# Performance work log

Hardware: AMD Instinct MI355X
Metric: run time of the kernel (lower is better)

Reference implementation:

```python
import jax, jax.numpy as jnp
import numpy as np

B, H, W, L, C = 4, 64, 64, 64, 64
NB, BS, F = 8, 8, 1          # num_blocks, block_size, hidden_size_factor
R, ALPHA = 8, 1.0            # lora_r, lora_alpha
M, T = 32, 8                 # modes, temporal_modes
SCALE = 1.0 / (BS * BS * F)  # param init scale from the module


def setup_inputs() -> dict:
    key = jax.random.key(0)
    ks = jax.random.split(key, 14)
    d = {"x": jax.random.normal(ks[0], (B, H, W, L, C), jnp.float32)}
    d["w1"] = SCALE * jax.random.uniform(ks[1], (2, NB, BS, BS * F), jnp.float32)
    d["b1"] = SCALE * jax.random.uniform(ks[2], (2, NB, BS * F), jnp.float32)
    d["w2"] = SCALE * jax.random.uniform(ks[3], (2, NB, BS * F, BS), jnp.float32)
    d["b2"] = SCALE * jax.random.uniform(ks[4], (2, NB, BS), jnp.float32)
    names = ["la1rA", "la1rB", "la1iA", "la1iB", "la2rA", "la2rB", "la2iA", "la2iB"]
    shapes = [(NB, BS, R), (NB, R, BS * F), (NB, BS, R), (NB, R, BS * F),
              (NB, BS * F, R), (NB, R, BS), (NB, BS * F, R), (NB, R, BS)]
    for i, (n, s) in enumerate(zip(names, shapes)):
        d[n] = 0.02 * jax.random.normal(ks[5 + i], s, jnp.float32)
    return d


def _afno(x, w1, b1, w2, b2, la1rA, la1rB, la1iA, la1iB, la2rA, la2rB, la2iA, la2iB):
    s = ALPHA / R
    # effective per-block weights: base + LoRA low-rank update  [NB, in, out]
    W1r = w1[0] + s * jnp.einsum('nir,nro->nio', la1rA, la1rB)
    W1i = w1[1] + s * jnp.einsum('nir,nro->nio', la1iA, la1iB)
    W2r = w2[0] + s * jnp.einsum('nir,nro->nio', la2rA, la2rB)
    W2i = w2[1] + s * jnp.einsum('nir,nro->nio', la2iA, la2iB)

    xf = jnp.fft.rfftn(x, axes=(1, 2, 3), norm='ortho')      # [B,H,W,L//2+1,C] complex
    Lh = xf.shape[3]
    xs = xf[:, :M, :M, :T].reshape(B, M, M, T, NB, BS)        # truncated modes, block split
    xr, xi = xs.real, xs.imag

    def lin(v, Wb, bb):  # block-diagonal linear: [...,n,i] x [n,i,o] + [n,o]
        return jnp.einsum('bxyzni,nio->bxyzno', v, Wb) + bb

    gelu = lambda t: jax.nn.gelu(t, approximate=False)
    o1r = gelu(lin(xr, W1r, b1[0]) - lin(xi, W1i, b1[1]))
    o1i = gelu(lin(xi, W1r, b1[0]) + lin(xr, W1i, b1[1]))
    o2r = lin(o1r, W2r, b2[0]) - lin(o1i, W2i, b2[1])
    o2i = lin(o1i, W2r, b2[0]) + lin(o1r, W2i, b2[1])

    o2 = (o2r + 1j * o2i).reshape(B, M, M, T, C)
    full = jnp.zeros((B, H, W, Lh, C), dtype=xf.dtype).at[:, :M, :M, :T].set(o2)
    out = jnp.fft.irfftn(full, s=(H, W, L), axes=(1, 2, 3), norm='ortho')
    return out + x


def reference(x, w1, b1, w2, b2, la1rA, la1rB, la1iA, la1iB, la2rA, la2rB, la2iA, la2iB):
    return _afno(x, w1, b1, w2, b2, la1rA, la1rB, la1iA, la1iB, la2rA, la2rB, la2iA, la2iB)
```

## Files before the change

kernel.cpp:

```cpp
#include <hip/hip_runtime.h>
#include <math.h>


#define PI2_64 0.09817477042468103f

__device__ __forceinline__ float gelu_exact(float t) {
    return 0.5f * t * (1.0f + erff(t * 0.7071067811865475f));
}

__global__ void __launch_bounds__(256) k1a_dft_l(const float* __restrict__ x,
                                                 float* __restrict__ y1f) {
    __shared__ float2 twT[8][64];
    int tid = threadIdx.x;
    {
        int k = tid >> 6, l = tid & 63;
        float s, c;
        sincosf(PI2_64 * (float)((k * l) & 63), &s, &c);
        twT[k][l] = make_float2(c, s);
        int k2 = k + 4;
        sincosf(PI2_64 * (float)((k2 * l) & 63), &s, &c);
        twT[k2][l] = make_float2(c, s);
    }
    __syncthreads();

    int bid = blockIdx.x;
    int w8 = bid & 7, bh = bid >> 3;
    int cp = tid & 31, wl = tid >> 5;
    int w = w8 * 8 + wl;
    const float* xp = x + (size_t)(bh * 64 + w) * 4096 + 2 * cp;

    float4 A[8];
#pragma unroll
    for (int kl = 0; kl < 8; ++kl) A[kl] = make_float4(0.f, 0.f, 0.f, 0.f);

    for (int l0 = 0; l0 < 64; l0 += 4) {
        float2 v0 = *(const float2*)(xp + (l0 + 0) * 64);
        float2 v1 = *(const float2*)(xp + (l0 + 1) * 64);
        float2 v2 = *(const float2*)(xp + (l0 + 2) * 64);
        float2 v3 = *(const float2*)(xp + (l0 + 3) * 64);
#pragma unroll
        for (int kl = 0; kl < 8; ++kl) {
            float2 t0 = twT[kl][l0 + 0];
            float2 t1 = twT[kl][l0 + 1];
            float2 t2 = twT[kl][l0 + 2];
            float2 t3 = twT[kl][l0 + 3];
            A[kl].x += v0.x * t0.x;  A[kl].y -= v0.x * t0.y;
            A[kl].z += v0.y * t0.x;  A[kl].w -= v0.y * t0.y;
            A[kl].x += v1.x * t1.x;  A[kl].y -= v1.x * t1.y;
            A[kl].z += v1.y * t1.x;  A[kl].w -= v1.y * t1.y;
            A[kl].x += v2.x * t2.x;  A[kl].y -= v2.x * t2.y;
            A[kl].z += v2.y * t2.x;  A[kl].w -= v2.y * t2.y;
            A[kl].x += v3.x * t3.x;  A[kl].y -= v3.x * t3.y;
            A[kl].z += v3.y * t3.x;  A[kl].w -= v3.y * t3.y;
        }
    }
    float4* y1 = (float4*)y1f;
    size_t base = (size_t)bh * 16384 + (size_t)w * 32 + cp;
#pragma unroll
    for (int kl = 0; kl < 8; ++kl)
        y1[base + kl * 2048] = A[kl];
}

__global__ void __launch_bounds__(256) k1b_dft_w(const float* __restrict__ y1f,
                                                 float* __restrict__ y2f) {
    __shared__ float4 sD[64 * 32];
    __shared__ float2 twT[32][64];
    int tid = threadIdx.x;
#pragma unroll
    for (int e = 0; e < 8; ++e) {
        int idx = e * 256 + tid;
        int k = idx >> 6, l = idx & 63;
        float s, c;
        sincosf(PI2_64 * (float)((k * l) & 63), &s, &c);
        twT[k][l] = make_float2(c, s);
    }
    int pos = blockIdx.x;
    int kl = pos & 7, bh = pos >> 3;
    const float4* src = (const float4*)y1f + (size_t)pos * 2048;
#pragma unroll
    for (int r = 0; r < 8; ++r)
        sD[r * 256 + tid] = src[r * 256 + tid];
    __syncthreads();

    int cp = tid & 31, kwg = tid >> 5;
    float4 acc[4];
#pragma unroll
    for (int i = 0; i < 4; ++i) acc[i] = make_float4(0.f, 0.f, 0.f, 0.f);

    for (int w = 0; w < 64; ++w) {
        float4 d = sD[w * 32 + cp];
#pragma unroll
        for (int i = 0; i < 4; ++i) {
            float2 t = twT[kwg * 4 + i][w];
            acc[i].x += d.x * t.x + d.y * t.y;
            acc[i].y += d.y * t.x - d.x * t.y;
            acc[i].z += d.z * t.x + d.w * t.y;
            acc[i].w += d.w * t.x - d.z * t.y;
        }
    }
    int b = bh >> 6, h = bh & 63;
    float4* y2 = (float4*)y2f;
#pragma unroll
    for (int i = 0; i < 4; ++i) {
        int kw = kwg * 4 + i;
        y2[((size_t)((b * 8 + kl) * 32 + kw) * 64 + h) * 32 + cp] = acc[i];
    }
}

__global__ void __launch_bounds__(256) kc_h_mlp(
        const float* __restrict__ y2f, float* __restrict__ z2f,
        const float* __restrict__ w1, const float* __restrict__ b1,
        const float* __restrict__ w2, const float* __restrict__ b2,
        const float* __restrict__ la1rA, const float* __restrict__ la1rB,
        const float* __restrict__ la1iA, const float* __restrict__ la1iB,
        const float* __restrict__ la2rA, const float* __restrict__ la2rB,
        const float* __restrict__ la2iA, const float* __restrict__ la2iB) {
    __shared__ float2 sD[64][64];
    __shared__ float2 sT[64][34];
    __shared__ float2 sM[32][66];
    __shared__ float  sW[4][512];
    __shared__ float  sb1[128], sb2[128];
    int tid = threadIdx.x;
    int pos = blockIdx.x;
    int kl = pos & 7, kw = (pos >> 3) & 31, b = pos >> 8;

#pragma unroll
    for (int r = 0; r < 8; ++r) {
        int idx = r * 256 + tid;
        int h = idx >> 5, kh = idx & 31;
        float sn, cs;
        sincosf(PI2_64 * (float)((h * kh) & 63), &sn, &cs);
        sT[h][kh] = make_float2(cs, -sn);
    }
    const float2* src = (const float2*)y2f + (size_t)((b * 8 + kl) * 32 + kw) * 4096;
#pragma unroll
    for (int r = 0; r < 8; ++r) {
        int f = r * 512 + tid * 2;
        *(float4*)(&sD[f >> 6][f & 63]) = *(const float4*)(src + f);
    }
    {
        const float* As[4]   = {la1rA, la1iA, la2rA, la2iA};
        const float* Bs[4]   = {la1rB, la1iB, la2rB, la2iB};
        const float* base[4] = {w1, w1 + 512, w2, w2 + 512};
#pragma unroll
        for (int e = 0; e < 8; ++e) {
            int flat = tid + e * 256;
            int mat = flat >> 9;
            int rem = flat & 511;
            int n = rem >> 6, i = (rem >> 3) & 7, o = rem & 7;
            const float* A  = As[mat] + n * 64 + i * 8;
            const float* Bp = Bs[mat] + n * 64 + o;
            float s = 0.f;
#pragma unroll
            for (int r = 0; r < 8; ++r) s += A[r] * Bp[r * 8];
            sW[mat][(i * 8 + o) * 8 + n] = base[mat][n * 64 + i * 8 + o] + 0.125f * s;
        }
        if (tid < 128) sb1[tid] = b1[tid];
        else           sb2[tid - 128] = b2[tid - 128];
    }
    __syncthreads();

    {
        int kh0 = (tid >> 5) * 4;
        int c0  = (tid & 31) * 2;
        float mr[4][2], mi[4][2];
#pragma unroll
        for (int i = 0; i < 4; ++i)
#pragma unroll
            for (int j = 0; j < 2; ++j) { mr[i][j] = 0.f; mi[i][j] = 0.f; }
        for (int h = 0; h < 64; ++h) {
            const float4* tT = (const float4*)(&sT[h][kh0]);
            float4 u0 = tT[0], u1 = tT[1];
            float4 d0 = *(const float4*)(&sD[h][c0]);
            float Tr[4] = {u0.x, u0.z, u1.x, u1.z};
            float Ti[4] = {u0.y, u0.w, u1.y, u1.w};
            float Dr[2] = {d0.x, d0.z};
            float Di[2] = {d0.y, d0.w};
#pragma unroll
            for (int i = 0; i < 4; ++i)
#pragma unroll
                for (int j = 0; j < 2; ++j) {
                    mr[i][j] += Tr[i] * Dr[j] - Ti[i] * Di[j];
                    mi[i][j] += Tr[i] * Di[j] + Ti[i] * Dr[j];
                }
        }
        const float sc = 1.0f / 512.0f;
#pragma unroll
        for (int i = 0; i < 4; ++i)
#pragma unroll
            for (int j = 0; j < 2; ++j)
                sM[kh0 + i][c0 + j] = make_float2(mr[i][j] * sc, mi[i][j] * sc);
    }
    __syncthreads();

    float2* sM2 = (float2*)&sD[0][0];
    {
        int kh = tid >> 3, n = tid & 7;
        float xr[8], xi[8];
#pragma unroll
        for (int i = 0; i < 8; ++i) {
            float2 v = sM[kh][n * 8 + i];
            xr[i] = v.x; xi[i] = v.y;
        }
        float o1r[8], o1i[8];
#pragma unroll
        for (int o = 0; o < 8; ++o) {
            float br = sb1[n * 8 + o], bi = sb1[64 + n * 8 + o];
            float sr = br - bi, si = br + bi;
#pragma unroll
            for (int i = 0; i < 8; ++i) {
                float wr = sW[0][(i * 8 + o) * 8 + n];
                float wi = sW[1][(i * 8 + o) * 8 + n];
                sr += xr[i] * wr - xi[i] * wi;
                si += xi[i] * wr + xr[i] * wi;
            }
            o1r[o] = gelu_exact(sr);
            o1i[o] = gelu_exact(si);
        }
#pragma unroll
        for (int o = 0; o < 8; ++o) {
            float br = sb2[n * 8 + o], bi = sb2[64 + n * 8 + o];
            float sr = br - bi, si = br + bi;
#pragma unroll
            for (int i = 0; i < 8; ++i) {
                float wr = sW[2][(i * 8 + o) * 8 + n];
                float wi = sW[3][(i * 8 + o) * 8 + n];
                sr += o1r[i] * wr - o1i[i] * wi;
                si += o1i[i] * wr + o1r[i] * wi;
            }
            sM2[kh * 66 + n * 8 + o] = make_float2(sr, si);
        }
    }
    __syncthreads();

    {
        int h0 = (tid >> 4) * 4;
        int c0 = (tid & 15) * 4;
        float orr[4][4], oii[4][4];
#pragma unroll
        for (int i = 0; i < 4; ++i)
#pragma unroll
            for (int j = 0; j < 4; ++j) { orr[i][j] = 0.f; oii[i][j] = 0.f; }
        for (int kh = 0; kh < 32; ++kh) {
            float2 T0 = sT[h0 + 0][kh];
            float2 T1 = sT[h0 + 1][kh];
            float2 T2 = sT[h0 + 2][kh];
            float2 T3 = sT[h0 + 3][kh];
            float Tr[4] = {T0.x, T1.x, T2.x, T3.x};
            float Ti[4] = {T0.y, T1.y, T2.y, T3.y};
            const float4* tM = (const float4*)(sM2 + kh * 66 + c0);
            float4 m0 = tM[0], m1 = tM[1];
            float Mr[4] = {m0.x, m0.z, m1.x, m1.z};
            float Mi[4] = {m0.y, m0.w, m1.y, m1.w};
#pragma unroll
            for (int i = 0; i < 4; ++i)
#pragma unroll
                for (int j = 0; j < 4; ++j) {
                    orr[i][j] += Tr[i] * Mr[j] + Ti[i] * Mi[j];
                    oii[i][j] += Tr[i] * Mi[j] - Ti[i] * Mr[j];
                }
        }
        float2* dst = (float2*)z2f + (size_t)((b * 8 + kl) * 32 + kw) * 4096;
#pragma unroll
        for (int i = 0; i < 4; ++i) {
            float4* d4 = (float4*)(dst + (h0 + i) * 64 + c0);
            d4[0] = make_float4(orr[i][0], oii[i][0], orr[i][1], oii[i][1]);
            d4[1] = make_float4(orr[i][2], oii[i][2], orr[i][3], oii[i][3]);
        }
    }
}

__global__ void __launch_bounds__(1024, 4) k3_wl(const float* __restrict__ x,
                                                 const float* __restrict__ z2f,
                                                 float* __restrict__ outp) {
    __shared__ float4 sZ[8 * 32 * 16];
    __shared__ float2 twA[8][64];
    int tid = threadIdx.x;
    int bid = blockIdx.x;
    int b = bid >> 7, h = (bid >> 1) & 63, ch = bid & 1;
    int c0 = ch * 32;

    if (tid < 512) {
        int k = tid >> 6, l = tid & 63;
        float s, c;
        sincosf(PI2_64 * (float)((k * l) & 63), &s, &c);
        twA[k][l] = make_float2(c, s);
    }
    const float4* z2 = (const float4*)z2f;
#pragma unroll
    for (int k = 0; k < 4; ++k) {
        int idx = k * 1024 + tid;
        int klkw = idx >> 4, cp = idx & 15;
        sZ[idx] = z2[(size_t)((b * 256 + klkw) * 64 + h) * 32 + ch * 16 + cp];
    }
    __syncthreads();

    int cp = tid & 15, w = tid >> 4;

    float4 zw[8];
#pragma unroll
    for (int kl = 0; kl < 8; ++kl) zw[kl] = make_float4(0.f, 0.f, 0.f, 0.f);
    float2 u = make_float2(1.f, 0.f);
    float2 su;
    {
        float s, c;
        sincosf(PI2_64 * (float)w, &s, &c);
        su = make_float2(c, s);
    }
    for (int kw = 0; kw < 32; ++kw) {
#pragma unroll
        for (int kl = 0; kl < 8; ++kl) {
            float4 d = sZ[(kl * 32 + kw) * 16 + cp];
            zw[kl].x += d.x * u.x - d.y * u.y;
            zw[kl].y += d.y * u.x + d.x * u.y;
            zw[kl].z += d.z * u.x - d.w * u.y;
            zw[kl].w += d.w * u.x + d.z * u.y;
        }
        float nr = u.x * su.x - u.y * su.y;
        float ni = u.y * su.x + u.x * su.y;
        u = make_float2(nr, ni);
    }

    float z0r0 = zw[0].x, z0r1 = zw[0].z;
#pragma unroll
    for (int kl = 1; kl < 8; ++kl) {
        zw[kl].x *= 2.f; zw[kl].y *= 2.f; zw[kl].z *= 2.f; zw[kl].w *= 2.f;
    }
    const float* xp = x + ((size_t)((b * 64 + h) * 64 + w) * 64) * 64 + c0 + 2 * cp;
    float* op = outp + ((size_t)((b * 64 + h) * 64 + w) * 64) * 64 + c0 + 2 * cp;
    const float sc = 1.0f / 512.0f;

    float2 xv0 = *(const float2*)(xp + 0 * 64);
    float2 xv1 = *(const float2*)(xp + 1 * 64);
    float2 xv2 = *(const float2*)(xp + 2 * 64);
    float2 xv3 = *(const float2*)(xp + 3 * 64);
    for (int l0 = 0; l0 < 64; l0 += 4) {
        int lp = (l0 + 4) & 63;
        float2 nx0 = *(const float2*)(xp + (lp + 0) * 64);
        float2 nx1 = *(const float2*)(xp + (lp + 1) * 64);
        float2 nx2 = *(const float2*)(xp + (lp + 2) * 64);
        float2 nx3 = *(const float2*)(xp + (lp + 3) * 64);
#pragma unroll
        for (int li = 0; li < 4; ++li) {
            int l = l0 + li;
            float s0 = z0r0, s1 = z0r1;
#pragma unroll
            for (int kl = 1; kl < 8; ++kl) {
                float2 t = twA[kl][l];
                s0 += zw[kl].x * t.x - zw[kl].y * t.y;
                s1 += zw[kl].z * t.x - zw[kl].w * t.y;
            }
            float2 xv = (li == 0) ? xv0 : (li == 1) ? xv1 : (li == 2) ? xv2 : xv3;
            *(float2*)(op + l * 64) = make_float2(s0 * sc + xv.x, s1 * sc + xv.y);
        }
        xv0 = nx0; xv1 = nx1; xv2 = nx2; xv3 = nx3;
    }
}

extern "C" void kernel_launch(void* const* d_in, const int* in_sizes, int n_in,
                              void* d_out, int out_size, void* d_ws, size_t ws_size,
                              hipStream_t stream) {
    const float* x     = (const float*)d_in[0];
    const float* w1    = (const float*)d_in[1];
    const float* b1    = (const float*)d_in[2];
    const float* w2    = (const float*)d_in[3];
    const float* b2    = (const float*)d_in[4];
    const float* la1rA = (const float*)d_in[5];
    const float* la1rB = (const float*)d_in[6];
    const float* la1iA = (const float*)d_in[7];
    const float* la1iB = (const float*)d_in[8];
    const float* la2rA = (const float*)d_in[9];
    const float* la2rB = (const float*)d_in[10];
    const float* la2iA = (const float*)d_in[11];
    const float* la2iB = (const float*)d_in[12];
    float* out = (float*)d_out;

    float* ws = (float*)d_ws;
    float* y1 = ws;
    float* y2 = ws + 16777216;
    float* z2 = ws + 25165824;

    hipLaunchKernelGGL(k1a_dft_l, dim3(2048), dim3(256),  0, stream, x, y1);
    hipLaunchKernelGGL(k1b_dft_w, dim3(2048), dim3(256),  0, stream, y1, y2);
    hipLaunchKernelGGL(kc_h_mlp,  dim3(1024), dim3(256),  0, stream, y2, z2,
                       w1, b1, w2, b2, la1rA, la1rB, la1iA, la1iB,
                       la2rA, la2rB, la2iA, la2iB);
    hipLaunchKernelGGL(k3_wl,     dim3(512),  dim3(1024), 0, stream, x, z2, out);
}
```

Before: 341.1 us.

## Split inverse W-DFT into even/odd kw halves, each thread computes w and w+32

The final inverse-DFT kernel now has each thread accumulate the even and odd kw frequency terms separately. Their sum gives output row w and their difference gives row w+32, since the twiddle for an odd kw flips sign when w shifts by 32. This halves the thread count per block and reuses each thread's shared-memory reads and twiddle work for two output rows. The cost is more registers per thread and fewer threads to hide global memory latency.

```diff
diff --git a/kernel.cpp b/kernel.cpp
--- a/kernel.cpp
+++ b/kernel.cpp
@@ -270,9 +270,9 @@
     }
 }
 
-__global__ void __launch_bounds__(1024, 4) k3_wl(const float* __restrict__ x,
-                                                 const float* __restrict__ z2f,
-                                                 float* __restrict__ outp) {
+__global__ void __launch_bounds__(512, 4) k3_wl(const float* __restrict__ x,
+                                                const float* __restrict__ z2f,
+                                                float* __restrict__ outp) {
     __shared__ float4 sZ[8 * 32 * 16];
     __shared__ float2 twA[8][64];
     int tid = threadIdx.x;
@@ -280,7 +280,7 @@
     int b = bid >> 7, h = (bid >> 1) & 63, ch = bid & 1;
     int c0 = ch * 32;
 
-    if (tid < 512) {
+    {
         int k = tid >> 6, l = tid & 63;
         float s, c;
         sincosf(PI2_64 * (float)((k * l) & 63), &s, &c);
@@ -288,72 +288,98 @@
     }
     const float4* z2 = (const float4*)z2f;
 #pragma unroll
-    for (int k = 0; k < 4; ++k) {
-        int idx = k * 1024 + tid;
+    for (int k = 0; k < 8; ++k) {
+        int idx = k * 512 + tid;
         int klkw = idx >> 4, cp = idx & 15;
         sZ[idx] = z2[(size_t)((b * 256 + klkw) * 64 + h) * 32 + ch * 16 + cp];
     }
     __syncthreads();
 
-    int cp = tid & 15, w = tid >> 4;
-
-    float4 zw[8];
-#pragma unroll
-    for (int kl = 0; kl < 8; ++kl) zw[kl] = make_float4(0.f, 0.f, 0.f, 0.f);
+    int cp = tid & 15, wlo = tid >> 4;
+
+    float4 zE[8], zO[8];
+#pragma unroll
+    for (int kl = 0; kl < 8; ++kl) {
+        zE[kl] = make_float4(0.f, 0.f, 0.f, 0.f);
+        zO[kl] = make_float4(0.f, 0.f, 0.f, 0.f);
+    }
     float2 u = make_float2(1.f, 0.f);
     float2 su;
     {
         float s, c;
-        sincosf(PI2_64 * (float)w, &s, &c);
+        sincosf(PI2_64 * (float)wlo, &s, &c);
         su = make_float2(c, s);
     }
-    for (int kw = 0; kw < 32; ++kw) {
+    for (int kw = 0; kw < 32; kw += 2) {
 #pragma unroll
         for (int kl = 0; kl < 8; ++kl) {
             float4 d = sZ[(kl * 32 + kw) * 16 + cp];
-            zw[kl].x += d.x * u.x - d.y * u.y;
-            zw[kl].y += d.y * u.x + d.x * u.y;
-            zw[kl].z += d.z * u.x - d.w * u.y;
-            zw[kl].w += d.w * u.x + d.z * u.y;
-        }
-        float nr = u.x * su.x - u.y * su.y;
-        float ni = u.y * su.x + u.x * su.y;
-        u = make_float2(nr, ni);
-    }
-
-    float z0r0 = zw[0].x, z0r1 = zw[0].z;
+            zE[kl].x += d.x * u.x - d.y * u.y;
+            zE[kl].y += d.y * u.x + d.x * u.y;
+            zE[kl].z += d.z * u.x - d.w * u.y;
+            zE[kl].w += d.w * u.x + d.z * u.y;
+        }
+        {
+            float nr = u.x * su.x - u.y * su.y;
+            float ni = u.y * su.x + u.x * su.y;
+            u = make_float2(nr, ni);
+        }
+#pragma unroll
+        for (int kl = 0; kl < 8; ++kl) {
+            float4 d = sZ[(kl * 32 + kw + 1) * 16 + cp];
+            zO[kl].x += d.x * u.x - d.y * u.y;
+            zO[kl].y += d.y * u.x + d.x * u.y;
+            zO[kl].z += d.z * u.x - d.w * u.y;
+            zO[kl].w += d.w * u.x + d.z * u.y;
+        }
+        {
+            float nr = u.x * su.x - u.y * su.y;
+            float ni = u.y * su.x + u.x * su.y;
+            u = make_float2(nr, ni);
+        }
+    }
+#pragma unroll
+    for (int kl = 0; kl < 8; ++kl) {
+        float4 e = zE[kl], o = zO[kl];
+        zE[kl] = make_float4(e.x + o.x, e.y + o.y, e.z + o.z, e.w + o.w);
+        zO[kl] = make_float4(e.x - o.x, e.y - o.y, e.z - o.z, e.w - o.w);
+    }
+
+    float zAr0 = zE[0].x, zAr1 = zE[0].z;
+    float zBr0 = zO[0].x, zBr1 = zO[0].z;
 #pragma unroll
     for (int kl = 1; kl < 8; ++kl) {
-        zw[kl].x *= 2.f; zw[kl].y *= 2.f; zw[kl].z *= 2.f; zw[kl].w *= 2.f;
-    }
-    const float* xp = x + ((size_t)((b * 64 + h) * 64 + w) * 64) * 64 + c0 + 2 * cp;
-    float* op = outp + ((size_t)((b * 64 + h) * 64 + w) * 64) * 64 + c0 + 2 * cp;
+        zE[kl].x *= 2.f; zE[kl].y *= 2.f; zE[kl].z *= 2.f; zE[kl].w *= 2.f;
+        zO[kl].x *= 2.f; zO[kl].y *= 2.f; zO[kl].z *= 2.f; zO[kl].w *= 2.f;
+    }
+    const size_t rowA = (size_t)((b * 64 + h) * 64 + wlo) * 4096;
+    const size_t rowB = rowA + (size_t)32 * 4096;
+    const float* xpA = x + rowA + c0 + 2 * cp;
+    const float* xpB = x + rowB + c0 + 2 * cp;
+    float* opA = outp + rowA + c0 + 2 * cp;
+    float* opB = outp + rowB + c0 + 2 * cp;
     const float sc = 1.0f / 512.0f;
 
-    float2 xv0 = *(const float2*)(xp + 0 * 64);
-    float2 xv1 = *(const float2*)(xp + 1 * 64);
-    float2 xv2 = *(const float2*)(xp + 2 * 64);
-    float2 xv3 = *(const float2*)(xp + 3 * 64);
-    for (int l0 = 0; l0 < 64; l0 += 4) {
-        int lp = (l0 + 4) & 63;
-        float2 nx0 = *(const float2*)(xp + (lp + 0) * 64);
-        float2 nx1 = *(const float2*)(xp + (lp + 1) * 64);
-        float2 nx2 = *(const float2*)(xp + (lp + 2) * 64);
-        float2 nx3 = *(const float2*)(xp + (lp + 3) * 64);
-#pragma unroll
-        for (int li = 0; li < 4; ++li) {
-            int l = l0 + li;
-            float s0 = z0r0, s1 = z0r1;
-#pragma unroll
-            for (int kl = 1; kl < 8; ++kl) {
-                float2 t = twA[kl][l];
-                s0 += zw[kl].x * t.x - zw[kl].y * t.y;
-                s1 += zw[kl].z * t.x - zw[kl].w * t.y;
-            }
-            float2 xv = (li == 0) ? xv0 : (li == 1) ? xv1 : (li == 2) ? xv2 : xv3;
-            *(float2*)(op + l * 64) = make_float2(s0 * sc + xv.x, s1 * sc + xv.y);
-        }
-        xv0 = nx0; xv1 = nx1; xv2 = nx2; xv3 = nx3;
+    float2 a0 = *(const float2*)(xpA + 0 * 64);
+    float2 b0 = *(const float2*)(xpB + 0 * 64);
+    float2 a1 = *(const float2*)(xpA + 1 * 64);
+    float2 b1 = *(const float2*)(xpB + 1 * 64);
+    for (int l = 0; l < 64; ++l) {
+        int lp = (l + 2) & 63;
+        float2 a2 = *(const float2*)(xpA + lp * 64);
+        float2 b2 = *(const float2*)(xpB + lp * 64);
+        float s0 = zAr0, s1 = zAr1, s2 = zBr0, s3 = zBr1;
+#pragma unroll
+        for (int kl = 1; kl < 8; ++kl) {
+            float2 t = twA[kl][l];
+            s0 += zE[kl].x * t.x - zE[kl].y * t.y;
+            s1 += zE[kl].z * t.x - zE[kl].w * t.y;
+            s2 += zO[kl].x * t.x - zO[kl].y * t.y;
+            s3 += zO[kl].z * t.x - zO[kl].w * t.y;
+        }
+        *(float2*)(opA + l * 64) = make_float2(s0 * sc + a0.x, s1 * sc + a0.y);
+        *(float2*)(opB + l * 64) = make_float2(s2 * sc + b0.x, s3 * sc + b0.y);
+        a0 = a1; a1 = a2; b0 = b1; b1 = b2;
     }
 }
 
@@ -380,10 +406,10 @@
     float* y2 = ws + 16777216;
     float* z2 = ws + 25165824;
 
-    hipLaunchKernelGGL(k1a_dft_l, dim3(2048), dim3(256),  0, stream, x, y1);
-    hipLaunchKernelGGL(k1b_dft_w, dim3(2048), dim3(256),  0, stream, y1, y2);
-    hipLaunchKernelGGL(kc_h_mlp,  dim3(1024), dim3(256),  0, stream, y2, z2,
+    hipLaunchKernelGGL(k1a_dft_l, dim3(2048), dim3(256), 0, stream, x, y1);
+    hipLaunchKernelGGL(k1b_dft_w, dim3(2048), dim3(256), 0, stream, y1, y2);
+    hipLaunchKernelGGL(kc_h_mlp,  dim3(1024), dim3(256), 0, stream, y2, z2,
                        w1, b1, w2, b2, la1rA, la1rB, la1iA, la1iB,
                        la2rA, la2rB, la2iA, la2iB);
-    hipLaunchKernelGGL(k3_wl,     dim3(512),  dim3(1024), 0, stream, x, z2, out);
-}
+    hipLaunchKernelGGL(k3_wl,     dim3(512),  dim3(512), 0, stream, x, z2, out);
+}
```

After: 338.1 us. About the same (-0.9%).
